# Performance work log

Measured on AMD Instinct MI355X. Metric: run time of the kernel, lower is better.

The kernel has to match this reference:

```python
import jax, jax.numpy as jnp
import numpy as np
from jax import lax

DN = ('NCHW', 'OIHW', 'NCHW')


def _conv(x, w, b, stride, pad):
    y = lax.conv_general_dilated(x, w, (stride, stride), [(pad, pad), (pad, pad)],
                                 dimension_numbers=DN)
    return y + b[None, :, None, None]


def _deconv(x, w, b, stride, pad):
    # torch ConvTranspose2d weight: (in, out, kH, kW). Equivalent forward conv:
    # flip spatially, swap in/out, dilate input by stride, pad by k-1-pad.
    k = w.shape[2]
    kern = jnp.flip(w, (2, 3)).transpose(1, 0, 2, 3)  # (out, in, kH, kW)
    p = k - 1 - pad
    y = lax.conv_general_dilated(x, kern, (1, 1), [(p, p), (p, p)],
                                 lhs_dilation=(stride, stride), dimension_numbers=DN)
    return y + b[None, :, None, None]


def setup_inputs() -> dict:
    key = jax.random.key(0)
    ks = jax.random.split(key, 16)
    s = 0.05
    D, K, H = 64, 512, 128  # embedding_dim, num_embeddings, hidden_channels
    inp = {
        'x': jax.random.uniform(ks[0], (16, 3, 256, 256), dtype=jnp.float32),
        'conv1_w': jax.random.normal(ks[1], (H, 3, 4, 4), jnp.float32) * s,
        'conv1_b': jnp.zeros((H,), jnp.float32),
        'conv2_w': jax.random.normal(ks[2], (H, H, 4, 4), jnp.float32) * s,
        'conv2_b': jnp.zeros((H,), jnp.float32),
        'conv3_w': jax.random.normal(ks[3], (D, H, 3, 3), jnp.float32) * s,
        'conv3_b': jnp.zeros((D,), jnp.float32),
        'emb': jax.random.normal(ks[4], (K, D), jnp.float32),
        'deconv1_w': jax.random.normal(ks[5], (D, H, 4, 4), jnp.float32) * s,
        'deconv1_b': jnp.zeros((H,), jnp.float32),
        'deconv2_w': jax.random.normal(ks[6], (H, H, 4, 4), jnp.float32) * s,
        'deconv2_b': jnp.zeros((H,), jnp.float32),
        'deconv3_w': jax.random.normal(ks[7], (H, 3, 3, 3), jnp.float32) * s,
        'deconv3_b': jnp.zeros((3,), jnp.float32),
    }
    return inp


def reference(x, conv1_w, conv1_b, conv2_w, conv2_b, conv3_w, conv3_b, emb,
              deconv1_w, deconv1_b, deconv2_w, deconv2_b, deconv3_w, deconv3_b):
    # Encoder
    h = jax.nn.relu(_conv(x, conv1_w, conv1_b, 2, 1))
    h = jax.nn.relu(_conv(h, conv2_w, conv2_b, 2, 1))
    z_e = _conv(h, conv3_w, conv3_b, 1, 1)  # (B, 64, 64, 64)

    # Vector quantizer (faithful to torch: flatten NCHW directly to (-1, D))
    D = emb.shape[1]
    flat = z_e.reshape(-1, D)  # (N, D)
    d = (jnp.sum(flat * flat, axis=1, keepdims=True)
         + jnp.sum(emb * emb, axis=1)
         - 2.0 * flat @ emb.T)  # (N, K)
    indices = jnp.argmin(d, axis=1)[:, None]  # (N, 1)
    z_q = emb[indices[:, 0]].reshape(z_e.shape)

    # Decoder
    g = jax.nn.relu(_deconv(z_q, deconv1_w, deconv1_b, 2, 1))
    g = jax.nn.relu(_deconv(g, deconv2_w, deconv2_b, 2, 1))
    x_recon = jax.nn.sigmoid(_deconv(g, deconv3_w, deconv3_b, 1, 1))
    return (x_recon, indices, z_q)
```

## Files before the change

### kernel.cpp

```cpp
#include <hip/hip_runtime.h>
#include <hip/hip_bf16.h>

#define DEV __device__ __forceinline__

typedef __attribute__((ext_vector_type(8))) short bf16x8;
typedef __attribute__((ext_vector_type(4))) float f32x4;
typedef __attribute__((ext_vector_type(4))) unsigned short u16x4;

#define MFMA16(a,b,c) __builtin_amdgcn_mfma_f32_16x16x32_bf16(a,b,c,0,0,0)

DEV unsigned short bfbits(float v){ __hip_bfloat16 h = __float2bfloat16(v); return *(unsigned short*)&h; }
DEV float bf2f(unsigned short u){ __hip_bfloat16 h = *(__hip_bfloat16*)&u; return __bfloat162float(h); }
DEV void split3(float v, unsigned short& h, unsigned short& m, unsigned short& l) {
  h = bfbits(v);        float r  = v - bf2f(h);
  m = bfbits(r);        float r2 = r - bf2f(m);
  l = bfbits(r2);
}
DEV uint4 zero4(){ uint4 z; z.x=0; z.y=0; z.z=0; z.w=0; return z; }
DEV void gload_lds16(const void* g, void* l) {
  __builtin_amdgcn_global_load_lds(
      (const __attribute__((address_space(1))) void*)g,
      (__attribute__((address_space(3))) void*)l, 16, 0, 0);
}

DEV void prep_deconv_img(int i, int CI, const float* __restrict__ w, unsigned short* __restrict__ w2) {
  const int nch = CI/16;
  int cil = i & 7, s = (i >> 3) & 7, co = (i >> 6) & 127, f = (i >> 13) & 1;
  int rest = i >> 14;
  int ch = rest % nch, e = rest / nch;
  int k = ch*64 + s*8 + cil;
  int ci = (k & 15) | ((k >> 6) << 4);
  int tap = (k >> 4) & 3, a = tap >> 1, b = tap & 1;
  float v = w[ (((long)ci*128 + co)*4 + (2*a+1-e))*4 + (2*b+1-f) ];
  w2[(long)(e*nch + ch)*16384 + ((long)(f*128 + co))*64 + ((s ^ (co&7))*8) + cil] = bfbits(v);
}
__global__ __launch_bounds__(256) void wprep_all(
    const float* __restrict__ c1w, float* __restrict__ w2c1,
    const float* __restrict__ c2w, unsigned short* __restrict__ w2c2,
    const float* __restrict__ c3w, unsigned short* __restrict__ w2c3,
    const float* __restrict__ d1w, unsigned short* __restrict__ w2d1,
    const float* __restrict__ d2w, unsigned short* __restrict__ w2d2,
    const float* __restrict__ d3w, unsigned short* __restrict__ w2d3,
    const float* __restrict__ emb, float* __restrict__ esq) {
  const int bx = blockIdx.x, t = threadIdx.x;
  if (bx < 24) {
    int i = bx*256 + t;
    if (i < 6144) {
      int tap = i & 15, ci = (i>>4) % 3, co = i / 48;
      w2c1[((long)ci*16 + tap)*128 + co] = c1w[i];
    }
  } else if (bx < 1048) {
    int i = (bx-24)*256 + t;
    int cil = i & 7, s = (i>>3) & 15, co = (i>>7) & 63;
    int ch = (i>>13) & 15, cog = i >> 17;
    int co_g = cog*64 + co, ci = ch*8 + cil, ky = s >> 2, kx = s & 3;
    float v = c2w[(((long)co_g*128 + ci)*4 + ky)*4 + kx];
    unsigned short h,m,l; split3(v,h,m,l);
    long base = (long)(cog*16 + ch)*24576 + ((long)co*16 + (s ^ (co&15)))*8 + cil;
    w2c2[base] = h; w2c2[base + 8192] = m; w2c2[base + 16384] = l;
  } else if (bx < 1432) {
    int i = (bx-1048)*256 + t;
    int k = i % 1536, co = i / 1536;
    int ch = k / 96, rem = k % 96;
    int tap = rem >> 3, cil = rem & 7;
    int ci = ch*8 + cil, ky = tap >> 2, kx = tap & 3;
    float v = (kx < 3) ? c3w[(((long)co*128 + ci)*3 + ky)*3 + kx] : 0.f;
    unsigned short h,m,l; split3(v,h,m,l);
    long base = (long)ch*24576 + ((long)co*16 + (tap ^ (co&15)))*8 + cil;
    w2c3[base] = h; w2c3[base + 8192] = m; w2c3[base + 16384] = l;
  } else if (bx < 1944) {
    prep_deconv_img((bx-1432)*256 + t, 64, d1w, w2d1);
  } else if (bx < 2968) {
    prep_deconv_img((bx-1944)*256 + t, 128, d2w, w2d2);
  } else if (bx < 3064) {
    int i = (bx-2968)*256 + t;
    if (i < 24576) {
      int k = i % 1536, co = i / 1536;
      int ch = k / 96, rem = k % 96;
      int tap = rem >> 3, cil = rem & 7;
      int ci = ch*8 + cil, ky = tap >> 2, kx = tap & 3;
      float v = (co < 3 && kx < 3) ? d3w[(((long)ci*3 + co)*3 + ky)*3 + kx] : 0.f;
      w2d3[i] = bfbits(v);
    }
  } else {
    int code = (bx-3064)*256 + t;
    if (code < 512) {
      const float4* ev = (const float4*)(emb + (long)code*64);
      float s = 0.f;
      #pragma unroll
      for (int q=0;q<16;q++){ float4 e4 = ev[q];
        s += e4.x*e4.x + e4.y*e4.y + e4.z*e4.z + e4.w*e4.w; }
      esq[code] = s;
    }
  }
}

__global__ __launch_bounds__(256) void conv1_split(
    const float* __restrict__ x, const float* __restrict__ w2,
    const float* __restrict__ bias, unsigned short* __restrict__ h1, long PS1) {
  __shared__ __align__(16) float sIn[3][18][20];
  __shared__ __align__(16) float sW[3*16*64];
  const int tid = threadIdx.x;
  const int b = blockIdx.z >> 1, cog = blockIdx.z & 1;
  const int co0 = cog*64;
  const int oy0 = blockIdx.y*8, ox0 = blockIdx.x*8;
  const int cg2 = tid >> 5;
  const int pg2 = tid & 31;
  const int r = pg2 >> 2, pxp = (pg2 & 3)*2;
  float acc[8][2];
  #pragma unroll
  for (int c=0;c<8;c++){ float bv = bias[co0 + cg2*8 + c];
    acc[c][0]=bv; acc[c][1]=bv; }
  const float* xb = x + (long)b*3*256*256;
  const int iy0 = 2*oy0 - 1, ix0 = 2*ox0 - 1;
  for (int t=tid; t<3*18*18; t+=256) {
    int xx = t%18, yy=(t/18)%18, ci=t/324;
    int gy = iy0+yy, gx = ix0+xx;
    float v = 0.f;
    if (gy>=0 && gy<256 && gx>=0 && gx<256) v = xb[((long)ci*256+gy)*256+gx];
    sIn[ci][yy][xx] = v;
  }
  for (int t=tid; t<3*16*64; t+=256) {
    sW[t] = w2[(long)(t>>6)*128 + co0 + (t&63)];
  }
  __syncthreads();
  for (int ci=0; ci<3; ci++) {
    #pragma unroll
    for (int ky=0;ky<4;ky++)
    #pragma unroll
    for (int kx=0;kx<4;kx++) {
      const float* wp = &sW[(ci*16 + ky*4+kx)*64 + cg2*8];
      float4 w0 = *(const float4*)wp;
      float4 w1 = *(const float4*)(wp+4);
      const int yy = 2*r + ky;
      #pragma unroll
      for (int p=0;p<2;p++) {
        float iv = sIn[ci][yy][2*(pxp+p)+kx];
        acc[0][p] += w0.x*iv; acc[1][p] += w0.y*iv;
        acc[2][p] += w0.z*iv; acc[3][p] += w0.w*iv;
        acc[4][p] += w1.x*iv; acc[5][p] += w1.y*iv;
        acc[6][p] += w1.z*iv; acc[7][p] += w1.w*iv;
      }
    }
  }
  const int chg = cog*8 + cg2;
  #pragma unroll
  for (int p=0;p<2;p++) {
    unsigned short th[8], tm[8], tl[8];
    #pragma unroll
    for (int c=0;c<8;c++) {
      float v = fmaxf(acc[c][p], 0.f);
      split3(v, th[c], tm[c], tl[c]);
    }
    long base = (((long)(b*128 + oy0+r)*16 + chg)*128 + ox0+pxp+p)*8;
    *(uint4*)(h1 + base)          = *(uint4*)th;
    *(uint4*)(h1 + PS1 + base)    = *(uint4*)tm;
    *(uint4*)(h1 + 2*PS1 + base)  = *(uint4*)tl;
  }
}

__global__ __launch_bounds__(256, 2) void conv2_mfma(
    const unsigned short* __restrict__ h1, long PS1,
    const unsigned short* __restrict__ w2,
    const float* __restrict__ bias,
    unsigned short* __restrict__ h2I) {
  __shared__ __align__(16) unsigned short sA[3][4][130][8];
  __shared__ __align__(16) unsigned short sB[24576];
  const int tid = threadIdx.x;
  const int oy = blockIdx.x, cog = blockIdx.y, b = blockIdx.z;
  const int wave = tid >> 6, lane = tid & 63;
  const int wr = wave >> 1, wc = wave & 1;
  const int col_l = lane & 15, kg = lane >> 4;
  const int iy0 = 2*oy - 1;
  f32x4 acc[2][2] = {};
  unsigned short* sAf = &sA[0][0][0][0];
  const unsigned short* bsrc = w2 + (long)cog*16*24576;

  int aOff[6], aLdsO[6]; bool aOk[6];
  #pragma unroll
  for (int j = 0; j < 6; ++j) {
    int idx = tid + j*256;
    int px = idx & 127, rr = (idx >> 7) & 3, pl = idx >> 9;
    int iy = iy0 + rr;
    aOk[j] = (iy >= 0 && iy < 128);
    aOff[j] = (int)(pl*PS1 + (long)(b*128 + (aOk[j]?iy:0))*16384 + px*8);
    aLdsO[j] = ((pl*4 + rr)*130 + px + 1)*8;
  }
  uint4 pA[6];
  #pragma unroll
  for (int j=0;j<6;j++)  pA[j] = aOk[j] ? *(const uint4*)(h1 + aOff[j]) : zero4();

  if (tid < 24) {
    int pl = tid>>3, rr=(tid>>1)&3, c=tid&1;
    *(uint4*)&sA[pl][rr][c?129:0][0] = zero4();
  }

  for (int ch = 0; ch < 16; ++ch) {
    __syncthreads();
    #pragma unroll
    for (int j=0;j<6;j++)  *(uint4*)(sAf + aLdsO[j]) = pA[j];
    #pragma unroll
    for (int j = 0; j < 12; ++j) {
      int blk = wave*12 + j;
      gload_lds16(bsrc + (long)ch*24576 + blk*512 + lane*8, &sB[blk*512]);
    }
    if (ch < 15) {
      #pragma unroll
      for (int j=0;j<6;j++)  pA[j] = aOk[j] ? *(const uint4*)(h1 + aOff[j] + (ch+1)*1024) : zero4();
    }
    __syncthreads();
    #pragma unroll
    for (int s = 0; s < 4; ++s) {
      bf16x8 aF[2][3]; bf16x8 bF[2][3];
      const int tap = s*4 + kg;
      #pragma unroll
      for (int mf = 0; mf < 2; ++mf) {
        int ox = wr*32 + mf*16 + col_l;
        #pragma unroll
        for (int pl = 0; pl < 3; ++pl)
          aF[mf][pl] = *(const bf16x8*)&sA[pl][s][2*ox + kg][0];
      }
      #pragma unroll
      for (int nf = 0; nf < 2; ++nf) {
        int co = wc*32 + nf*16 + col_l;
        int ba = (co*16 + (tap ^ (co&15)))*8;
        bF[nf][0] = *(const bf16x8*)&sB[ba];
        bF[nf][1] = *(const bf16x8*)&sB[ba + 8192];
        bF[nf][2] = *(const bf16x8*)&sB[ba + 16384];
      }
      __builtin_amdgcn_s_setprio(1);
      #pragma unroll
      for (int mf = 0; mf < 2; ++mf)
      #pragma unroll
      for (int nf = 0; nf < 2; ++nf) {
        f32x4 a = acc[mf][nf];
        a = MFMA16(aF[mf][0], bF[nf][0], a);
        a = MFMA16(aF[mf][0], bF[nf][1], a);
        a = MFMA16(aF[mf][1], bF[nf][0], a);
        a = MFMA16(aF[mf][0], bF[nf][2], a);
        a = MFMA16(aF[mf][2], bF[nf][0], a);
        a = MFMA16(aF[mf][1], bF[nf][1], a);
        acc[mf][nf] = a;
      }
      __builtin_amdgcn_s_setprio(0);
    }
  }
  __syncthreads();
  #pragma unroll
  for (int nf = 0; nf < 2; ++nf) {
    int co = wc*32 + nf*16 + col_l;
    float bv = bias[cog*64 + co];
    #pragma unroll
    for (int mf = 0; mf < 2; ++mf) {
      int px0 = wr*32 + mf*16 + kg*4;
      u16x4 oh, om, ol;
      #pragma unroll
      for (int r = 0; r < 4; ++r) {
        float v = fmaxf(acc[mf][nf][r] + bv, 0.f);
        unsigned short h,m,l; split3(v,h,m,l);
        oh[r]=h; om[r]=m; ol[r]=l;
      }
      *(u16x4*)&sB[(0*64 + co)*72 + px0] = oh;
      *(u16x4*)&sB[(1*64 + co)*72 + px0] = om;
      *(u16x4*)&sB[(2*64 + co)*72 + px0] = ol;
    }
  }
  __syncthreads();
  #pragma unroll
  for (int j = 0; j < 6; ++j) {
    int idx = tid + j*256;
    int pl = idx >> 9, ch = (idx >> 6) & 7, px = idx & 63;
    unsigned short tmp[8];
    #pragma unroll
    for (int c = 0; c < 8; ++c) tmp[c] = sB[(pl*64 + ch*8 + c)*72 + px];
    *(uint4*)(h2I + ((((long)(b*64 + oy)*3 + pl)*16 + cog*8 + ch)*64 + px)*8) = *(uint4*)tmp;
  }
}

__global__ __launch_bounds__(256, 2) void conv3_mfma(
    const unsigned short* __restrict__ h2I,
    const unsigned short* __restrict__ w2,
    const float* __restrict__ bias,
    unsigned short* __restrict__ zeH, unsigned short* __restrict__ zeM,
    unsigned short* __restrict__ zeL) {
  __shared__ __align__(16) unsigned short sA3[3][3][68][8];
  __shared__ __align__(16) unsigned short sB[24576];
  const int tid = threadIdx.x;
  const int oy = blockIdx.x, b = blockIdx.z;
  const int wave = tid >> 6, lane = tid & 63;
  const int wr = wave >> 1, wc = wave & 1;
  const int col_l = lane & 15, kg = lane >> 4;
  f32x4 acc[2][2] = {};
  if (tid < 27) {
    int row = tid/3, c = tid%3;
    int pl = row/3, rr = row%3;
    *(uint4*)&sA3[pl][rr][(c==0)?0:(64+c)][0] = zero4();
  }
  if (oy == 0 && tid < 192) {
    int pl = tid >> 6, px = tid & 63;
    *(uint4*)&sA3[pl][0][px+1][0] = zero4();
  }
  if (oy == 63 && tid < 192) {
    int pl = tid >> 6, px = tid & 63;
    *(uint4*)&sA3[pl][2][px+1][0] = zero4();
  }

  for (int ch = 0; ch < 16; ++ch) {
    __syncthreads();
    #pragma unroll
    for (int j = 0; j < 3; ++j) {
      int row = wave*3 + j;
      if (row < 9) {
        int pl = row/3, rr = row%3;
        int iy = oy + rr - 1;
        if (iy >= 0 && iy < 64)
          gload_lds16(h2I + ((((long)(b*64 + iy)*3 + pl)*16 + ch)*64)*8 + lane*8,
                      &sA3[pl][rr][1][0]);
      }
    }
    #pragma unroll
    for (int j = 0; j < 12; ++j) {
      int blk = wave*12 + j;
      gload_lds16(w2 + (long)ch*24576 + blk*512 + lane*8, &sB[blk*512]);
    }
    __syncthreads();
    #pragma unroll
    for (int s = 0; s < 3; ++s) {
      bf16x8 aF[2][3]; bf16x8 bF[2][3];
      const int tap = s*4 + kg;
      #pragma unroll
      for (int mf = 0; mf < 2; ++mf) {
        int ox = wr*32 + mf*16 + col_l;
        #pragma unroll
        for (int pl = 0; pl < 3; ++pl)
          aF[mf][pl] = *(const bf16x8*)&sA3[pl][s][ox + kg][0];
      }
      #pragma unroll
      for (int nf = 0; nf < 2; ++nf) {
        int co = wc*32 + nf*16 + col_l;
        int ba = (co*16 + (tap ^ (co&15)))*8;
        bF[nf][0] = *(const bf16x8*)&sB[ba];
        bF[nf][1] = *(const bf16x8*)&sB[ba + 8192];
        bF[nf][2] = *(const bf16x8*)&sB[ba + 16384];
      }
      __builtin_amdgcn_s_setprio(1);
      #pragma unroll
      for (int mf = 0; mf < 2; ++mf)
      #pragma unroll
      for (int nf = 0; nf < 2; ++nf) {
        f32x4 a = acc[mf][nf];
        a = MFMA16(aF[mf][0], bF[nf][0], a);
        a = MFMA16(aF[mf][0], bF[nf][1], a);
        a = MFMA16(aF[mf][1], bF[nf][0], a);
        a = MFMA16(aF[mf][0], bF[nf][2], a);
        a = MFMA16(aF[mf][2], bF[nf][0], a);
        a = MFMA16(aF[mf][1], bF[nf][1], a);
        acc[mf][nf] = a;
      }
      __builtin_amdgcn_s_setprio(0);
    }
  }
  __syncthreads();
  #pragma unroll
  for (int nf = 0; nf < 2; ++nf) {
    int co = wc*32 + nf*16 + col_l;
    float bv = bias[co];
    #pragma unroll
    for (int mf = 0; mf < 2; ++mf) {
      int px0 = wr*32 + mf*16 + kg*4;
      u16x4 oh, om, ol;
      #pragma unroll
      for (int r = 0; r < 4; ++r) {
        float v = acc[mf][nf][r] + bv;
        unsigned short h,m,l; split3(v,h,m,l);
        oh[r]=h; om[r]=m; ol[r]=l;
      }
      *(u16x4*)&sB[(0*64 + co)*72 + px0] = oh;
      *(u16x4*)&sB[(1*64 + co)*72 + px0] = om;
      *(u16x4*)&sB[(2*64 + co)*72 + px0] = ol;
    }
  }
  __syncthreads();
  #pragma unroll
  for (int j = 0; j < 6; ++j) {
    int idx = tid + j*256;
    int pl = idx >> 9, co_l = (idx >> 3) & 63, q = idx & 7;
    uint4 v = *(const uint4*)&sB[(pl*64 + co_l)*72 + q*8];
    unsigned short* dst = (pl==0) ? zeH : ((pl==1) ? zeM : zeL);
    *(uint4*)(dst + ((long)(b*64 + co_l)*64 + oy)*64 + q*8) = v;
  }
}

template<int TX, int MODE>
struct SmemD {
  union {
    struct { __align__(16) unsigned short In[2][TX+2][24];
             __align__(16) unsigned short W[2*128*64]; } o;
    struct { __align__(16) unsigned short In[2][TX+2][16];
             __align__(16) unsigned short W[2*128*64]; } v;
    __align__(16) unsigned short Out[2*TX][136];
  };
};

template<int CIN, int TX, int MODE>
__global__ __launch_bounds__(TX*4, (TX==64)?3:4) void deconv_mfma(
    const void* __restrict__ xin, const unsigned short* __restrict__ w2,
    const float* __restrict__ bias, unsigned short* __restrict__ yI) {
  constexpr int NTHR = TX*4;
  constexpr int NWAVE = NTHR/64;
  constexpr int NWG  = 32/NWAVE;
  __shared__ SmemD<TX,MODE> sm;
  unsigned short* Wb = MODE ? &sm.v.W[0] : &sm.o.W[0];

  const int tid = threadIdx.x;
  const int ty = blockIdx.x, e = blockIdx.y, b = blockIdx.z;
  const int wave = tid >> 6, lane = tid & 63;
  const int wc = wave & 1, wr = wave >> 1;
  const int f = (wr*64) / TX;
  const int tx_base = (wr*64) & (TX-1);
  const int col_l = lane & 15, kg = lane >> 4;
  const unsigned short* wsrc = w2 + (long)e*(CIN/16)*16384;

  constexpr int TPR = NTHR/32;
  const int rowid = tid / TPR, liO = tid % TPR;
  const int sci = rowid >> 1, srr = rowid & 1;
  float4 pLo, pHi; uint4 pIn;
  long aBase = 0; bool aOk = false;
  int pxV = 0, halfV = 0, rrV = 0;
  if (MODE == 0) {
    int iy = ty + e - 1 + srr;
    aOk = (iy >= 0 && iy < TX);
    aBase = ((long)b*CIN + sci)*TX*TX + (long)(aOk?iy:0)*TX + liO*8;
    if (aOk) { const float4* s4 = (const float4*)((const float*)xin + aBase);
               pLo = s4[0]; pHi = s4[1]; }
  } else {
    halfV = tid & 1; pxV = (tid >> 1) & (TX-1); rrV = tid >> 8;
    int iy = ty + e - 1 + rrV;
    aOk = (iy >= 0 && iy < TX);
    aBase = ((long)b*TX + (aOk?iy:0))*((long)(CIN/8)*TX*8) + (long)halfV*TX*8 + pxV*8;
    pIn = aOk ? *(const uint4*)((const unsigned short*)xin + aBase) : zero4();
  }

  if (MODE == 0) {
    if (tid < 64) {
      int rr = tid & 1, cc = ((tid>>1)&1) ? TX+1 : 0, ci = tid >> 2;
      sm.o.In[rr][cc][ci] = 0;
    }
  } else {
    if (tid < 8) {
      int rr = tid & 1, c = (tid>>1)&1, hf = (tid>>2)&1;
      *(uint4*)&sm.v.In[rr][c?TX+1:0][hf*8] = zero4();
    }
  }

  f32x4 acc[4][4] = {};
  for (int ch = 0; ch < CIN/16; ++ch) {
    __syncthreads();
    if (MODE == 0) {
      unsigned short vals[8];
      if (aOk) {
        float4 lo = pLo, hi = pHi;
        vals[0]=bfbits(lo.x); vals[1]=bfbits(lo.y); vals[2]=bfbits(lo.z); vals[3]=bfbits(lo.w);
        vals[4]=bfbits(hi.x); vals[5]=bfbits(hi.y); vals[6]=bfbits(hi.z); vals[7]=bfbits(hi.w);
      } else {
        #pragma unroll
        for (int j=0;j<8;j++) vals[j] = 0;
      }
      #pragma unroll
      for (int j=0;j<8;j++) {
        int jj = (j + liO) & 7;
        sm.o.In[srr][1 + liO*8 + jj][sci] = vals[jj];
      }
    } else {
      *(uint4*)&sm.v.In[rrV][pxV+1][halfV*8] = pIn;
    }
    #pragma unroll
    for (int j = 0; j < NWG; ++j) {
      int blk = wave*NWG + j;
      gload_lds16(wsrc + (long)ch*16384 + blk*512 + lane*8, Wb + blk*512);
    }
    if (ch + 1 < CIN/16) {
      if (MODE == 0) {
        if (aOk) { const float4* s4 = (const float4*)((const float*)xin + aBase + (long)(ch+1)*16*TX*TX);
                   pLo = s4[0]; pHi = s4[1]; }
      } else {
        pIn = aOk ? *(const uint4*)((const unsigned short*)xin + aBase + (ch+1)*2*TX*8) : zero4();
      }
    }
    __syncthreads();
    #pragma unroll
    for (int kk = 0; kk < 2; ++kk) {
      bf16x8 aF[4];
      const int tap = kk*2 + (kg >> 1), a = tap >> 1, bb = tap & 1;
      #pragma unroll
      for (int mf = 0; mf < 4; ++mf) {
        int tx = tx_base + mf*16 + col_l;
        if (MODE == 0) aF[mf] = *(const bf16x8*)&sm.o.In[1-a][tx + 1 + f - bb][(kg&1)*8];
        else           aF[mf] = *(const bf16x8*)&sm.v.In[1-a][tx + 1 + f - bb][(kg&1)*8];
      }
      const int slot = kk*4 + kg;
      __builtin_amdgcn_s_setprio(1);
      #pragma unroll
      for (int nf = 0; nf < 4; ++nf) {
        int co_l = nf*16 + col_l;
        bf16x8 bF = *(const bf16x8*)(Wb + (f*128 + wc*64 + co_l)*64 + (slot ^ (co_l & 7))*8);
        #pragma unroll
        for (int mf = 0; mf < 4; ++mf)
          acc[mf][nf] = MFMA16(aF[mf], bF, acc[mf][nf]);
      }
      __builtin_amdgcn_s_setprio(0);
    }
  }

  __syncthreads();
  float bv[4];
  #pragma unroll
  for (int nf = 0; nf < 4; ++nf) bv[nf] = bias[wc*64 + nf*16 + col_l];
  #pragma unroll
  for (int mf = 0; mf < 4; ++mf)
  #pragma unroll
  for (int nf = 0; nf < 4; ++nf) {
    int co = wc*64 + nf*16 + col_l;
    #pragma unroll
    for (int r = 0; r < 4; ++r) {
      int tx = tx_base + mf*16 + kg*4 + r;
      float v = fmaxf(acc[mf][nf][r] + bv[nf], 0.f);
      int ox = 2*tx + f;
      sm.Out[ox][co ^ (((ox>>3)&7)<<3)] = bfbits(v);
    }
  }
  __syncthreads();
  const int oy = 2*ty + e;
  #pragma unroll
  for (int j = 0; j < 8; ++j) {
    int i = tid + j*NTHR;
    int px = i & (2*TX-1), chn = i / (2*TX);
    uint4 vv = *(const uint4*)&sm.Out[px][(chn*8) ^ (((px>>3)&7)<<3)];
    *(uint4*)(yI + ((((long)b*(2*TX) + oy)*16 + chn)*(2*TX) + px)*8) = vv;
  }
}

__global__ __launch_bounds__(256, 2) void deconv3_mfma(
    const unsigned short* __restrict__ g2I,
    const unsigned short* __restrict__ w2,
    const float* __restrict__ bias, float* __restrict__ y) {
  __shared__ __align__(16) unsigned short sA[3][260][8];
  __shared__ __align__(16) unsigned short sB[16*12*16*8];
  const int tid = threadIdx.x;
  const int oy = blockIdx.x, b = blockIdx.y;
  const int wave = tid >> 6, lane = tid & 63;
  const int col_l = lane & 15, kg = lane >> 4;
  const int pxb = wave*64;
  for (int i = tid; i < 3072; i += 256) {
    int co = i & 15, tap = (i>>4) % 12, ch = i/192;
    *(uint4*)&sB[((ch*12+tap)*16+co)*8] = *(const uint4*)(w2 + (long)co*1536 + ch*96 + tap*8);
  }
  if (tid < 12) {
    int dy = tid >> 2, c = tid & 3;
    *(uint4*)&sA[dy][(c<2)?c:(256+c)][0] = zero4();
  }
  long aBase[3]; int aLdsO[3]; bool aOk[3];
  #pragma unroll
  for (int u = 0; u < 3; ++u) {
    int idx = tid + u*256;
    int px = idx & 255, dy = idx >> 8;
    int iy = oy - 1 + dy;
    aOk[u] = (iy >= 0 && iy < 256);
    aBase[u] = ((long)(b*256 + (aOk[u]?iy:0)))*32768 + px*8;
    aLdsO[u] = (dy*260 + px + 2)*8;
  }
  uint4 pA[3];
  #pragma unroll
  for (int u=0;u<3;u++) pA[u] = aOk[u] ? *(const uint4*)(g2I + aBase[u]) : zero4();

  unsigned short* sAf = &sA[0][0][0];
  f32x4 acc[4] = {};
  for (int ch = 0; ch < 16; ++ch) {
    __syncthreads();
    #pragma unroll
    for (int u=0;u<3;u++) *(uint4*)(sAf + aLdsO[u]) = pA[u];
    if (ch < 15) {
      #pragma unroll
      for (int u=0;u<3;u++)
        pA[u] = aOk[u] ? *(const uint4*)(g2I + aBase[u] + (ch+1)*2048) : zero4();
    }
    __syncthreads();
    #pragma unroll
    for (int s = 0; s < 3; ++s) {
      bf16x8 bF = *(const bf16x8*)&sB[((ch*12 + s*4 + kg)*16 + col_l)*8];
      __builtin_amdgcn_s_setprio(1);
      #pragma unroll
      for (int mf = 0; mf < 4; ++mf) {
        int px = pxb + mf*16 + col_l;
        bf16x8 aF = *(const bf16x8*)&sA[2-s][px + 3 - kg][0];
        acc[mf] = MFMA16(aF, bF, acc[mf]);
      }
      __builtin_amdgcn_s_setprio(0);
    }
  }
  if (col_l < 3) {
    float bv = bias[col_l];
    #pragma unroll
    for (int mf = 0; mf < 4; ++mf) {
      int px = pxb + mf*16 + kg*4;
      float4 o;
      o.x = 1.f/(1.f + expf(-(acc[mf][0] + bv)));
      o.y = 1.f/(1.f + expf(-(acc[mf][1] + bv)));
      o.z = 1.f/(1.f + expf(-(acc[mf][2] + bv)));
      o.w = 1.f/(1.f + expf(-(acc[mf][3] + bv)));
      *(float4*)(y + ((long)(b*3 + col_l)*256 + oy)*256 + px) = o;
    }
  }
}

__global__ __launch_bounds__(256, 2) void vq_mfma(
    const unsigned short* __restrict__ zeH, const unsigned short* __restrict__ zeM,
    const unsigned short* __restrict__ zeL,
    const float* __restrict__ emb, const float* __restrict__ esq,
    float* __restrict__ out_idx, float* __restrict__ zq) {
  __shared__ __align__(16) unsigned short sA[64*3*8*8];
  __shared__ __align__(16) unsigned short sB[128*3*8*8];
  __shared__ float snb[128];
  __shared__ int sidx[64];
  const int tid = threadIdx.x;
  const long n0 = (long)blockIdx.x*64;
  const int wave = tid >> 6, lane = tid & 63;
  const int col = lane & 15, kg = lane >> 4;

  #pragma unroll
  for (int j = 0; j < 6; ++j) {
    int idx = tid + j*256;
    int pl = idx >> 9, rem = idx & 511;
    int n = rem >> 3, slot = rem & 7;
    const unsigned short* src = (pl==0 ? zeH : (pl==1 ? zeM : zeL)) + (n0+n)*64 + slot*8;
    *(uint4*)&sA[((n*3 + pl)*8 + (slot ^ (n&7)))*8] = *(const uint4*)src;
  }

  const int codeT = tid >> 1, halfT = tid & 1;
  float4 pB[8];
  #pragma unroll
  for (int q = 0; q < 8; ++q)
    pB[q] = *(const float4*)(emb + (long)codeT*64 + halfT*32 + q*4);
  float pSn = (tid < 128) ? esq[tid] : 0.f;

  float best[4] = {3.4e38f,3.4e38f,3.4e38f,3.4e38f};
  int bidx[4] = {0,0,0,0};

  for (int ch = 0; ch < 4; ++ch) {
    __syncthreads();
    #pragma unroll
    for (int s4 = 0; s4 < 4; ++s4) {
      int slot = halfT*4 + s4;
      float4 lo = pB[s4*2], hi = pB[s4*2+1];
      unsigned short th[8], tm[8], tl[8];
      split3(lo.x, th[0], tm[0], tl[0]); split3(lo.y, th[1], tm[1], tl[1]);
      split3(lo.z, th[2], tm[2], tl[2]); split3(lo.w, th[3], tm[3], tl[3]);
      split3(hi.x, th[4], tm[4], tl[4]); split3(hi.y, th[5], tm[5], tl[5]);
      split3(hi.z, th[6], tm[6], tl[6]); split3(hi.w, th[7], tm[7], tl[7]);
      int base = ((codeT*3)*8 + (slot ^ (codeT&7)))*8;
      *(uint4*)&sB[base]       = *(uint4*)th;
      *(uint4*)&sB[base + 64]  = *(uint4*)tm;
      *(uint4*)&sB[base + 128] = *(uint4*)tl;
    }
    if (tid < 128) snb[tid] = pSn;
    if (ch < 3) {
      #pragma unroll
      for (int q = 0; q < 8; ++q)
        pB[q] = *(const float4*)(emb + ((long)(ch+1)*128 + codeT)*64 + halfT*32 + q*4);
      if (tid < 128) pSn = esq[(ch+1)*128 + tid];
    }
    __syncthreads();

    f32x4 acc[8] = {};
    #pragma unroll
    for (int kk = 0; kk < 2; ++kk) {
      const int nloc = wave*16 + col;
      const int slot = kk*4 + kg;
      bf16x8 aF[3];
      #pragma unroll
      for (int pl = 0; pl < 3; ++pl)
        aF[pl] = *(const bf16x8*)&sA[((nloc*3 + pl)*8 + (slot ^ (nloc&7)))*8];
      __builtin_amdgcn_s_setprio(1);
      #pragma unroll
      for (int cf = 0; cf < 8; ++cf) {
        int cl = cf*16 + col;
        int bb = ((cl*3)*8 + (slot ^ (cl&7)))*8;
        bf16x8 b0 = *(const bf16x8*)&sB[bb];
        bf16x8 b1 = *(const bf16x8*)&sB[bb + 64];
        bf16x8 b2 = *(const bf16x8*)&sB[bb + 128];
        f32x4 a = acc[cf];
        a = MFMA16(aF[0], b0, a);
        a = MFMA16(aF[0], b1, a);
        a = MFMA16(aF[1], b0, a);
        a = MFMA16(aF[0], b2, a);
        a = MFMA16(aF[2], b0, a);
        a = MFMA16(aF[1], b1, a);
        acc[cf] = a;
      }
      __builtin_amdgcn_s_setprio(0);
    }
    #pragma unroll
    for (int cf = 0; cf < 8; ++cf) {
      float sv = snb[cf*16 + col];
      int code = ch*128 + cf*16 + col;
      #pragma unroll
      for (int j = 0; j < 4; ++j) {
        float s = sv - 2.f*acc[cf][j];
        if (s < best[j]) { best[j] = s; bidx[j] = code; }
      }
    }
  }

  #pragma unroll
  for (int j = 0; j < 4; ++j) {
    float b = best[j]; int ii = bidx[j];
    #pragma unroll
    for (int off = 1; off < 16; off <<= 1) {
      float ob = __shfl_xor(b, off);
      int oi = __shfl_xor(ii, off);
      if (ob < b || (ob == b && oi < ii)) { b = ob; ii = oi; }
    }
    if (col == 0) sidx[wave*16 + kg*4 + j] = ii;
  }
  __syncthreads();
  if (tid < 64) out_idx[n0 + tid] = (float)sidx[tid];
  #pragma unroll
  for (int j = 0; j < 4; ++j) {
    int t = tid + j*256;
    int row = t >> 4, q = t & 15;
    float4 v = *(const float4*)(emb + (long)sidx[row]*64 + q*4);
    *(float4*)(zq + (n0 + row)*64 + q*4) = v;
  }
}

extern "C" void kernel_launch(void* const* d_in, const int* in_sizes, int n_in,
                              void* d_out, int out_size, void* d_ws, size_t ws_size,
                              hipStream_t stream) {
  const float* x   = (const float*)d_in[0];
  const float* c1w = (const float*)d_in[1];  const float* c1b = (const float*)d_in[2];
  const float* c2w = (const float*)d_in[3];  const float* c2b = (const float*)d_in[4];
  const float* c3w = (const float*)d_in[5];  const float* c3b = (const float*)d_in[6];
  const float* emb = (const float*)d_in[7];
  const float* d1w = (const float*)d_in[8];  const float* d1b = (const float*)d_in[9];
  const float* d2w = (const float*)d_in[10]; const float* d2b = (const float*)d_in[11];
  const float* d3w = (const float*)d_in[12]; const float* d3b = (const float*)d_in[13];
  float* out = (float*)d_out;

  float* xrec = out;
  float* oidx = out + 3145728;
  float* zq   = out + 3211264;

  const long XB  = 196608;
  const long ZEB = 262144;
  const long PS1 = 8388608;
  const long H2B = 1572864;

  const size_t NEEDED = 112273408ULL;
  if (ws_size < NEEDED) return;
  char* wsb = (char*)d_ws;
  unsigned short* h1grp = (unsigned short*)wsb;
  unsigned short* g2grp = (unsigned short*)wsb;
  unsigned short* h2I   = (unsigned short*)(wsb + 67108864);
  unsigned short* g1grp = (unsigned short*)(wsb + 67108864);
  unsigned short* zeH = (unsigned short*)(wsb + 92274688);
  unsigned short* zeM = (unsigned short*)(wsb + 100663296);
  unsigned short* zeL = (unsigned short*)out;
  char* W = wsb + 109051904;
  float* w2c1          = (float*)(W);
  unsigned short* w2c2 = (unsigned short*)(W + 24576);
  unsigned short* w2c3 = (unsigned short*)(W + 1597440);
  unsigned short* w2d1 = (unsigned short*)(W + 2383872);
  unsigned short* w2d2 = (unsigned short*)(W + 2646016);
  unsigned short* w2d3 = (unsigned short*)(W + 3170304);
  float* esq           = (float*)(W + 3219456);

  wprep_all<<<3066, 256, 0, stream>>>(c1w, w2c1, c2w, w2c2, c3w, w2c3,
                                      d1w, w2d1, d2w, w2d2, d3w, w2d3, emb, esq);

  for (int g = 0; g < 4; ++g) {
    conv1_split<<<dim3(16,16,8), 256, 0, stream>>>(
        x + (long)g*4*XB, w2c1, c1b, h1grp, PS1);
    conv2_mfma<<<dim3(64,2,4), 256, 0, stream>>>(
        h1grp, PS1, w2c2, c2b, h2I + (long)(g&1)*4*H2B);
    if (g & 1) {
      long zo = (long)(g>>1)*8*ZEB;
      conv3_mfma<<<dim3(64,1,8), 256, 0, stream>>>(
          h2I, w2c3, c3b, zeH + zo, zeM + zo, zeL + zo);
    }
  }
  vq_mfma<<<1024, 256, 0, stream>>>(zeH, zeM, zeL, emb, esq, oidx, zq);

  for (int g = 0; g < 4; ++g) {
    deconv_mfma<64, 64, 0 ><<<dim3(64, 2, 4), 256, 0, stream>>>(
        (const void*)(zq + (long)g*4*ZEB), w2d1, d1b, g1grp);
    deconv_mfma<128,128,1 ><<<dim3(128,2,4), 512, 0, stream>>>(
        (const void*)g1grp, w2d2, d2b, g2grp);
    deconv3_mfma<<<dim3(256,4), 256, 0, stream>>>(
        g2grp, w2d3, d3b, xrec + (long)g*4*XB);
  }
}
```

Before: 746.2 us.

## Shrink deconv output staging, raise occupancy, issue prefetch after barrier

```diff
diff --git a/kernel.cpp b/kernel.cpp
--- a/kernel.cpp
+++ b/kernel.cpp
@@ -204,11 +204,12 @@
       int blk = wave*12 + j;
       gload_lds16(bsrc + (long)ch*24576 + blk*512 + lane*8, &sB[blk*512]);
     }
+    __syncthreads();
     if (ch < 15) {
       #pragma unroll
       for (int j=0;j<6;j++)  pA[j] = aOk[j] ? *(const uint4*)(h1 + aOff[j] + (ch+1)*1024) : zero4();
-    }
-    __syncthreads();
+      __builtin_amdgcn_sched_barrier(0);
+    }
     #pragma unroll
     for (int s = 0; s < 4; ++s) {
       bf16x8 aF[2][3]; bf16x8 bF[2][3];
@@ -398,12 +399,12 @@
              __align__(16) unsigned short W[2*128*64]; } o;
     struct { __align__(16) unsigned short In[2][TX+2][16];
              __align__(16) unsigned short W[2*128*64]; } v;
-    __align__(16) unsigned short Out[2*TX][136];
+    __align__(16) unsigned short Out[128][136];
   };
 };
 
 template<int CIN, int TX, int MODE>
-__global__ __launch_bounds__(TX*4, (TX==64)?3:4) void deconv_mfma(
+__global__ __launch_bounds__(TX*4, (TX==64)?4:6) void deconv_mfma(
     const void* __restrict__ xin, const unsigned short* __restrict__ w2,
     const float* __restrict__ bias, unsigned short* __restrict__ yI) {
   constexpr int NTHR = TX*4;
@@ -479,6 +480,7 @@
       int blk = wave*NWG + j;
       gload_lds16(wsrc + (long)ch*16384 + blk*512 + lane*8, Wb + blk*512);
     }
+    __syncthreads();
     if (ch + 1 < CIN/16) {
       if (MODE == 0) {
         if (aOk) { const float4* s4 = (const float4*)((const float*)xin + aBase + (long)(ch+1)*16*TX*TX);
@@ -486,8 +488,8 @@
       } else {
         pIn = aOk ? *(const uint4*)((const unsigned short*)xin + aBase + (ch+1)*2*TX*8) : zero4();
       }
-    }
-    __syncthreads();
+      __builtin_amdgcn_sched_barrier(0);
+    }
     #pragma unroll
     for (int kk = 0; kk < 2; ++kk) {
       bf16x8 aF[4];
@@ -516,27 +518,59 @@
   float bv[4];
   #pragma unroll
   for (int nf = 0; nf < 4; ++nf) bv[nf] = bias[wc*64 + nf*16 + col_l];
-  #pragma unroll
-  for (int mf = 0; mf < 4; ++mf)
-  #pragma unroll
-  for (int nf = 0; nf < 4; ++nf) {
-    int co = wc*64 + nf*16 + col_l;
-    #pragma unroll
-    for (int r = 0; r < 4; ++r) {
-      int tx = tx_base + mf*16 + kg*4 + r;
-      float v = fmaxf(acc[mf][nf][r] + bv[nf], 0.f);
-      int ox = 2*tx + f;
-      sm.Out[ox][co ^ (((ox>>3)&7)<<3)] = bfbits(v);
-    }
-  }
-  __syncthreads();
   const int oy = 2*ty + e;
-  #pragma unroll
-  for (int j = 0; j < 8; ++j) {
-    int i = tid + j*NTHR;
-    int px = i & (2*TX-1), chn = i / (2*TX);
-    uint4 vv = *(const uint4*)&sm.Out[px][(chn*8) ^ (((px>>3)&7)<<3)];
-    *(uint4*)(yI + ((((long)b*(2*TX) + oy)*16 + chn)*(2*TX) + px)*8) = vv;
+  if constexpr (TX == 64) {
+    #pragma unroll
+    for (int mf = 0; mf < 4; ++mf)
+    #pragma unroll
+    for (int nf = 0; nf < 4; ++nf) {
+      int co = wc*64 + nf*16 + col_l;
+      #pragma unroll
+      for (int r = 0; r < 4; ++r) {
+        int tx = tx_base + mf*16 + kg*4 + r;
+        float v = fmaxf(acc[mf][nf][r] + bv[nf], 0.f);
+        int ox = 2*tx + f;
+        sm.Out[ox][co ^ (((ox>>3)&7)<<3)] = bfbits(v);
+      }
+    }
+    __syncthreads();
+    #pragma unroll
+    for (int j = 0; j < 8; ++j) {
+      int i = tid + j*NTHR;
+      int px = i & 127, chn = i >> 7;
+      uint4 vv = *(const uint4*)&sm.Out[px][(chn*8) ^ (((px>>3)&7)<<3)];
+      *(uint4*)(yI + ((((long)b*128 + oy)*16 + chn)*128 + px)*8) = vv;
+    }
+  } else {
+    const int myp = wr & 1;
+    #pragma unroll
+    for (int p = 0; p < 2; ++p) {
+      if (myp == p) {
+        #pragma unroll
+        for (int mf = 0; mf < 4; ++mf)
+        #pragma unroll
+        for (int nf = 0; nf < 4; ++nf) {
+          int co = wc*64 + nf*16 + col_l;
+          #pragma unroll
+          for (int r = 0; r < 4; ++r) {
+            int tx = tx_base + mf*16 + kg*4 + r;
+            float v = fmaxf(acc[mf][nf][r] + bv[nf], 0.f);
+            int ox = 2*tx + f;
+            sm.Out[ox & 127][co ^ (((ox>>3)&7)<<3)] = bfbits(v);
+          }
+        }
+      }
+      __syncthreads();
+      #pragma unroll
+      for (int j = 0; j < 4; ++j) {
+        int i = tid + j*NTHR;
+        int px = i & 127, chn = i >> 7;
+        uint4 vv = *(const uint4*)&sm.Out[px][(chn*8) ^ (((px>>3)&7)<<3)];
+        int pxg = p*128 + px;
+        *(uint4*)(yI + ((((long)b*256 + oy)*16 + chn)*256 + pxg)*8) = vv;
+      }
+      if (p == 0) __syncthreads();
+    }
   }
 }
 
@@ -579,12 +613,13 @@
     __syncthreads();
     #pragma unroll
     for (int u=0;u<3;u++) *(uint4*)(sAf + aLdsO[u]) = pA[u];
+    __syncthreads();
     if (ch < 15) {
       #pragma unroll
       for (int u=0;u<3;u++)
         pA[u] = aOk[u] ? *(const uint4*)(g2I + aBase[u] + (ch+1)*2048) : zero4();
-    }
-    __syncthreads();
+      __builtin_amdgcn_sched_barrier(0);
+    }
     #pragma unroll
     for (int s = 0; s < 3; ++s) {
       bf16x8 bF = *(const bf16x8*)&sB[((ch*12 + s*4 + kg)*16 + col_l)*8];
```

After: 2.284 ms. +206.0%, slower.
